# Kernel tuning notes

Hardware: AMD Instinct MI355X
Metric: run time of the kernel (lower is better)

## Reference

```python
import jax, jax.numpy as jnp
import numpy as np

N = 30000      # nodes
E = 300000     # edges (before self-loops)
F_NODE = 32; F_EDGE = 16
HID = 64       # hidden_channels
H = 4; C = 64  # heads, per-head channels (GATConv out_channels = HID)
NEG_SLOPE_ATT = 0.2   # GATConv negative_slope
NEG_SLOPE_ACT = 0.01  # F.leaky_relu default
LN_EPS = 1e-5


def setup_inputs() -> dict:
    key = jax.random.key(0)
    ks = jax.random.split(key, 32)
    def w(k, shape, fan_in):
        return jax.random.normal(k, shape, jnp.float32) * (1.0 / np.sqrt(fan_in))
    inp = {
        "x": jax.random.normal(ks[0], (N, F_NODE), jnp.float32),
        "edge_index": jax.random.randint(ks[1], (2, E), 0, N),
        "edge_attr": jax.random.normal(ks[2], (E, F_EDGE), jnp.float32),
        "wn": w(ks[3], (F_NODE, HID), F_NODE), "bn": jnp.zeros((HID,), jnp.float32),
        "we": w(ks[4], (F_EDGE, HID), F_EDGE), "be": jnp.zeros((HID,), jnp.float32),
    }
    for i, off in ((1, 5), (2, 13)):
        inp[f"lin{i}"] = w(ks[off], (HID, H * C), HID)        # GATConv.lin
        inp[f"line{i}"] = w(ks[off + 1], (HID, H * C), HID)    # GATConv.lin_edge
        inp[f"as{i}"] = w(ks[off + 2], (H, C), C)              # att_src
        inp[f"ad{i}"] = w(ks[off + 3], (H, C), C)              # att_dst
        inp[f"ae{i}"] = w(ks[off + 4], (H, C), C)              # att_edge
        inp[f"b{i}"] = jnp.zeros((C,), jnp.float32)            # GATConv bias (concat=False -> C)
        inp[f"g{i}"] = jnp.ones((HID,), jnp.float32)           # LayerNorm weight
        inp[f"bt{i}"] = jnp.zeros((HID,), jnp.float32)         # LayerNorm bias
    return inp


def layernorm(x, g, b):
    mu = x.mean(-1, keepdims=True)
    v = ((x - mu) ** 2).mean(-1, keepdims=True)
    return (x - mu) / jnp.sqrt(v + LN_EPS) * g + b


def gat_layer(x, src, dst, e_attr, lin_w, lin_e_w, att_src, att_dst, att_edge, bias, n):
    # x: [n, HID]; e_attr: [E2, HID]; edge lists already include self-loops
    E2 = src.shape[0]
    h = (x @ lin_w).reshape(n, H, C)          # [n,H,C]
    e = (e_attr @ lin_e_w).reshape(E2, H, C)  # [E2,H,C]
    a_src = (h * att_src[None]).sum(-1)       # [n,H]
    a_dst = (h * att_dst[None]).sum(-1)       # [n,H]
    a_edge = (e * att_edge[None]).sum(-1)     # [E2,H]
    a = jax.nn.leaky_relu(a_src[src] + a_dst[dst] + a_edge, NEG_SLOPE_ATT)
    # scatter-softmax over destination neighborhoods (every node has a self-loop)
    m = jax.ops.segment_max(a, dst, num_segments=n)
    ex = jnp.exp(a - m[dst])
    den = jax.ops.segment_sum(ex, dst, num_segments=n)
    alpha = ex / den[dst]                     # [E2,H]
    out = jax.ops.segment_sum(h[src] * alpha[..., None], dst, num_segments=n)  # [n,H,C]
    return out.mean(axis=1) + bias, alpha     # concat=False: average heads


def reference(x, edge_index, edge_attr, wn, bn, we, be,
              lin1, line1, as1, ad1, ae1, b1, g1, bt1,
              lin2, line2, as2, ad2, ae2, b2, g2, bt2):
    n = x.shape[0]
    x = jax.nn.relu(x @ wn + bn)
    ea = jax.nn.relu(edge_attr @ we + be)
    src, dst = edge_index[0], edge_index[1]
    # PyG add_self_loops(fill_value='mean'): self-loop edge_attr = mean of incoming edge_attr
    ones = jnp.ones((src.shape[0],), ea.dtype)
    deg = jax.ops.segment_sum(ones, dst, num_segments=n)
    mean_ea = jax.ops.segment_sum(ea, dst, num_segments=n) / jnp.maximum(deg, 1.0)[:, None]
    loop = jnp.arange(n, dtype=src.dtype)
    src_f = jnp.concatenate([src, loop])
    dst_f = jnp.concatenate([dst, loop])
    ea_f = jnp.concatenate([ea, mean_ea], axis=0)
    h1, alpha1 = gat_layer(x, src_f, dst_f, ea_f, lin1, line1, as1, ad1, ae1, b1, n)
    h1 = layernorm(jax.nn.leaky_relu(h1, NEG_SLOPE_ACT), g1, bt1)
    # dropout is identity in eval mode
    h2, alpha2 = gat_layer(h1, src_f, dst_f, ea_f, lin2, line2, as2, ad2, ae2, b2, n)
    h2 = layernorm(jax.nn.leaky_relu(h2, NEG_SLOPE_ACT), g2, bt2)
    return h2, alpha1, alpha2
```

## Files before the change

kernel.cpp:

```cpp
#include <hip/hip_runtime.h>

#define FN 32
#define FE 16
#define HID 64
#define HEADS 4
#define CHC 64

typedef float f32x4 __attribute__((ext_vector_type(4)));

__device__ __forceinline__ float bf2f(unsigned short u) {
  unsigned int x = ((unsigned int)u) << 16;
  return __builtin_bit_cast(float, x);
}
__device__ __forceinline__ unsigned short f2bf(float f) {
  unsigned int x = __builtin_bit_cast(unsigned int, f);
  unsigned int r = (x + 0x7fff + ((x >> 16) & 1)) >> 16;
  return (unsigned short)r;
}
__device__ __forceinline__ unsigned int pack2bf(float a, float b) {
  return (unsigned int)f2bf(a) | ((unsigned int)f2bf(b) << 16);
}

__device__ __forceinline__ void reduce8_store(const float p[8],
    float* __restrict__ arr1, float* __restrict__ arr2, size_t pos, int lane,
    float scale)
{
  float q[4];
  {
    bool hi = lane & 1;
    #pragma unroll
    for (int m = 0; m < 4; m++) {
      float keep = hi ? p[m + 4] : p[m];
      float send = hi ? p[m] : p[m + 4];
      q[m] = keep + __shfl_xor(send, 1);
    }
  }
  float r[2];
  {
    bool hi = lane & 2;
    #pragma unroll
    for (int m = 0; m < 2; m++) {
      float keep = hi ? q[m + 2] : q[m];
      float send = hi ? q[m] : q[m + 2];
      r[m] = keep + __shfl_xor(send, 2);
    }
  }
  float s;
  {
    bool hi = lane & 4;
    float keep = hi ? r[1] : r[0];
    float send = hi ? r[0] : r[1];
    s = keep + __shfl_xor(send, 4);
  }
  s += __shfl_xor(s, 8);
  s += __shfl_xor(s, 16);
  s += __shfl_xor(s, 32);
  if (lane < 8) {
    int entry = ((lane & 1) << 2) | (lane & 2) | ((lane >> 2) & 1);
    if (entry < 4) arr1[pos * 4 + entry] = s * scale;
    else           arr2[pos * 4 + entry - 4] = s * scale;
  }
}

__global__ __launch_bounds__(256) void k_vecs(
    const float* __restrict__ lin1, const float* __restrict__ line1,
    const float* __restrict__ as1, const float* __restrict__ ad1,
    const float* __restrict__ ae1,
    const float* __restrict__ lin2, const float* __restrict__ line2,
    const float* __restrict__ as2, const float* __restrict__ ad2,
    const float* __restrict__ ae2,
    float* __restrict__ vS, float* __restrict__ vD, float* __restrict__ vE)
{
  int bi = blockIdx.x;
  int l = bi / 3, kind = bi % 3;
  const float* lin = (kind == 2) ? (l ? line2 : line1) : (l ? lin2 : lin1);
  const float* att = (kind == 0) ? (l ? as2 : as1)
                   : (kind == 1) ? (l ? ad2 : ad1) : (l ? ae2 : ae1);
  float* out = ((kind == 0) ? vS : (kind == 1) ? vD : vE) + l * 256;
  int t = threadIdx.x;
  int c = t >> 2, hd = t & 3;
  float acc = 0.f;
  for (int cc = 0; cc < CHC; cc++)
    acc += lin[c * (HEADS * CHC) + hd * CHC + cc] * att[hd * CHC + cc];
  out[c * 4 + hd] = acc;
}

__global__ __launch_bounds__(256) void k_x1(const float* __restrict__ x,
    const float* __restrict__ wn, const float* __restrict__ bn,
    const float* __restrict__ vS, const float* __restrict__ vD,
    float* __restrict__ x1, float* __restrict__ ssrc, float* __restrict__ sdst,
    int n)
{
  int t = threadIdx.x; int w = t >> 6; int lane = t & 63;
  int v = blockIdx.x * 4 + w;
  __shared__ float xs[4][FN];
  if (v < n && lane < FN) xs[w][lane] = x[(size_t)v * FN + lane];
  __syncthreads();
  if (v >= n) return;
  float acc = bn[lane];
  #pragma unroll
  for (int k = 0; k < FN; k++) acc += xs[w][k] * wn[k * HID + lane];
  acc = fmaxf(acc, 0.f);
  x1[(size_t)v * HID + lane] = acc;
  float4 s4 = ((const float4*)vS)[lane];
  float4 d4 = ((const float4*)vD)[lane];
  float p[8] = {acc * s4.x, acc * s4.y, acc * s4.z, acc * s4.w,
                acc * d4.x, acc * d4.y, acc * d4.z, acc * d4.w};
  reduce8_store(p, ssrc, sdst, (size_t)v, lane, 1.f);
}

__global__ __launch_bounds__(256) void k_deg(const int* __restrict__ dst,
                                             int* __restrict__ deg, int E)
{
  int e = blockIdx.x * 256 + threadIdx.x;
  if (e < E) atomicAdd(&deg[dst[e]], 1);
}

__global__ __launch_bounds__(1024) void k_scan1(const int* __restrict__ deg,
    int* __restrict__ rowptr, int* __restrict__ bsum, int n)
{
  __shared__ int wsum[16];
  int t = threadIdx.x, wv = t >> 6, lane = t & 63;
  int i = blockIdx.x * 1024 + t;
  int val = (i < n) ? deg[i] : 0;
  int sc = val;
  #pragma unroll
  for (int off = 1; off < 64; off <<= 1) {
    int u = __shfl_up(sc, off);
    if (lane >= off) sc += u;
  }
  if (lane == 63) wsum[wv] = sc;
  __syncthreads();
  int woff = 0;
  #pragma unroll
  for (int k = 0; k < 16; k++) woff += (k < wv) ? wsum[k] : 0;
  if (i < n) rowptr[i] = woff + sc - val;
  if (t == 0) {
    int tot = 0;
    #pragma unroll
    for (int k = 0; k < 16; k++) tot += wsum[k];
    bsum[blockIdx.x] = tot;
  }
}

__global__ __launch_bounds__(1024) void k_scan23(const int* __restrict__ bsum,
    int* __restrict__ rowptr, int nb, int n)
{
  int b = blockIdx.x;
  int t = threadIdx.x;
  int off = 0;
  for (int j = 0; j < b; j++) off += bsum[j];
  int i = b * 1024 + t;
  if (i < n) rowptr[i] += off;
  if (b == 0 && t == 0) {
    int tot = 0;
    for (int j = 0; j < nb; j++) tot += bsum[j];
    rowptr[n] = tot;
  }
}

__global__ __launch_bounds__(256) void k_fill(const int* __restrict__ src,
    const int* __restrict__ dst, const int* __restrict__ rowptr,
    int* __restrict__ cnt, int* __restrict__ eid, int* __restrict__ srcs,
    int* __restrict__ perm, int E)
{
  int e = blockIdx.x * 256 + threadIdx.x;
  if (e < E) {
    int d = dst[e];
    int pos = rowptr[d] + atomicAdd(&cnt[d], 1);
    eid[pos] = e;
    srcs[pos] = src[e];
    perm[e] = pos;
  }
}

__global__ __launch_bounds__(256) void k_aeg_e(const float* __restrict__ eattr,
    const float* __restrict__ we, const float* __restrict__ be,
    const float* __restrict__ vE, const int* __restrict__ perm,
    float* __restrict__ aeg1, float* __restrict__ aeg2, int E)
{
  __shared__ float4 we_t4[HID][4];
  __shared__ float4 vE_s[2][HID];
  __shared__ float  be_s[HID];
  int t = threadIdx.x;
  for (int i = t; i < FE * HID; i += 256) {
    int k = i >> 6, c = i & 63;
    ((float*)we_t4)[c * 16 + k] = we[i];
  }
  for (int i = t; i < 512; i += 256) ((float*)vE_s)[i] = vE[i];
  if (t < HID) be_s[t] = be[t];
  __syncthreads();

  int e = blockIdx.x * 256 + t;
  if (e >= E) return;
  const float4* er = (const float4*)(eattr + (size_t)e * FE);
  float4 A = er[0], B = er[1], C4 = er[2], D = er[3];
  float ta[FE] = {A.x, A.y, A.z, A.w, B.x, B.y, B.z, B.w,
                  C4.x, C4.y, C4.z, C4.w, D.x, D.y, D.z, D.w};
  float4 acc1 = make_float4(0.f, 0.f, 0.f, 0.f);
  float4 acc2 = make_float4(0.f, 0.f, 0.f, 0.f);
  #pragma unroll 4
  for (int c = 0; c < HID; c++) {
    float4 w0 = we_t4[c][0], w1 = we_t4[c][1], w2 = we_t4[c][2], w3 = we_t4[c][3];
    float ea = be_s[c];
    ea += ta[0] * w0.x + ta[1] * w0.y + ta[2] * w0.z + ta[3] * w0.w;
    ea += ta[4] * w1.x + ta[5] * w1.y + ta[6] * w1.z + ta[7] * w1.w;
    ea += ta[8] * w2.x + ta[9] * w2.y + ta[10] * w2.z + ta[11] * w2.w;
    ea += ta[12] * w3.x + ta[13] * w3.y + ta[14] * w3.z + ta[15] * w3.w;
    ea = fmaxf(ea, 0.f);
    float4 u1 = vE_s[0][c], u2 = vE_s[1][c];
    acc1.x += ea * u1.x; acc1.y += ea * u1.y; acc1.z += ea * u1.z; acc1.w += ea * u1.w;
    acc2.x += ea * u2.x; acc2.y += ea * u2.y; acc2.z += ea * u2.z; acc2.w += ea * u2.w;
  }
  int pos = perm[e];
  *(float4*)(aeg1 + (size_t)pos * 4) = acc1;
  *(float4*)(aeg2 + (size_t)pos * 4) = acc2;
}

__global__ __launch_bounds__(256) void k_self_aeg(const int* __restrict__ rowptr,
    float* __restrict__ aeg1, float* __restrict__ aeg2, int E, int n)
{
  int t = threadIdx.x;
  int v = blockIdx.x * 32 + (t >> 3);
  if (v >= n) return;
  int ent = t & 7;
  int h = ent & 3;
  const float* srcp = (ent < 4) ? aeg1 : aeg2;
  int r0 = rowptr[v], r1 = rowptr[v + 1];
  float s = 0.f;
  for (int j = r0; j < r1; j++) s += srcp[(size_t)j * 4 + h];
  float m = s / fmaxf((float)(r1 - r0), 1.f);
  if (ent < 4) aeg1[((size_t)E + v) * 4 + h] = m;
  else         aeg2[((size_t)E + v) * 4 + h] = m;
}

__global__ __launch_bounds__(256) void k_h(const float* __restrict__ xin,
    const float* __restrict__ lin, unsigned short* __restrict__ h_bf, int n)
{
  int t = threadIdx.x, wv = t >> 6, lane = t & 63;
  int v0 = blockIdx.x * 16;
  __shared__ float xs[16][HID];
  {
    int node = t >> 4, ch4 = (t & 15) * 4;
    int vv = v0 + node;
    float4 val = make_float4(0.f, 0.f, 0.f, 0.f);
    if (vv < n) val = *(const float4*)(xin + (size_t)vv * HID + ch4);
    *(float4*)&xs[node][ch4] = val;
  }
  __syncthreads();
  float acc[4][4];
  #pragma unroll
  for (int i = 0; i < 4; i++)
    #pragma unroll
    for (int j = 0; j < 4; j++) acc[i][j] = 0.f;
  const float4* lin4 = (const float4*)lin;
  int nd0 = wv * 4;
  #pragma unroll 4
  for (int kb = 0; kb < 16; kb++) {
    float4 xv[4];
    #pragma unroll
    for (int i = 0; i < 4; i++) xv[i] = *(const float4*)&xs[nd0 + i][kb * 4];
    float4 lv0 = lin4[(kb * 4 + 0) * 64 + lane];
    float4 lv1 = lin4[(kb * 4 + 1) * 64 + lane];
    float4 lv2 = lin4[(kb * 4 + 2) * 64 + lane];
    float4 lv3 = lin4[(kb * 4 + 3) * 64 + lane];
    #pragma unroll
    for (int i = 0; i < 4; i++) {
      acc[i][0] += xv[i].x * lv0.x + xv[i].y * lv1.x + xv[i].z * lv2.x + xv[i].w * lv3.x;
      acc[i][1] += xv[i].x * lv0.y + xv[i].y * lv1.y + xv[i].z * lv2.y + xv[i].w * lv3.y;
      acc[i][2] += xv[i].x * lv0.z + xv[i].y * lv1.z + xv[i].z * lv2.z + xv[i].w * lv3.z;
      acc[i][3] += xv[i].x * lv0.w + xv[i].y * lv1.w + xv[i].z * lv2.w + xv[i].w * lv3.w;
    }
  }
  #pragma unroll
  for (int i = 0; i < 4; i++) {
    int v = v0 + nd0 + i;
    if (v < n) {
      uint2 u;
      u.x = pack2bf(acc[i][0], acc[i][1]);
      u.y = pack2bf(acc[i][2], acc[i][3]);
      *(uint2*)(h_bf + (size_t)v * 256 + lane * 4) = u;
    }
  }
}

template<bool DOTS>
__global__ __launch_bounds__(256) void k_node(
    const unsigned short* __restrict__ h_bf, const float* __restrict__ ssrc,
    const float* __restrict__ sdst, const float* __restrict__ aegc,
    const int* __restrict__ rowptr, const int* __restrict__ eidArr,
    const int* __restrict__ srcs, const float* __restrict__ bias,
    const float* __restrict__ gamma, const float* __restrict__ beta,
    const float* __restrict__ vS2, const float* __restrict__ vD2,
    float* __restrict__ alpha_out, float* __restrict__ xout,
    float* __restrict__ ssrc_o, float* __restrict__ sdst_o, int n, int E)
{
  __shared__ float als[4][4][64];
  __shared__ int   svec[4][64];
  int t = threadIdx.x; int wv = t >> 6, lane = t & 63;
  int v = blockIdx.x * 4 + wv;
  if (v >= n) return;
  int r0 = rowptr[v], r1 = rowptr[v + 1];
  int deg = r1 - r0, ne = deg + 1;
  int coff = lane * 4;
  int hh = lane >> 4;
  float acc0 = 0.f, acc1 = 0.f, acc2 = 0.f, acc3 = 0.f;
  const float4* aeg4 = (const float4*)aegc;
  const float4* ss4p = (const float4*)ssrc;
  float4 sd4 = ((const float4*)sdst)[v];

  if (ne <= 64) {
    int s = v, eo = E + v;
    if (lane < deg) { s = srcs[r0 + lane]; eo = eidArr[r0 + lane]; }
    bool valid = (lane < ne);
    float a0 = -INFINITY, a1 = -INFINITY, a2 = -INFINITY, a3 = -INFINITY;
    if (valid) {
      float4 ae4 = aeg4[(lane < deg) ? (r0 + lane) : (E + v)];
      float4 ss4 = ss4p[s];
      a0 = ss4.x + sd4.x + ae4.x; a0 = (a0 > 0.f) ? a0 : 0.2f * a0;
      a1 = ss4.y + sd4.y + ae4.y; a1 = (a1 > 0.f) ? a1 : 0.2f * a1;
      a2 = ss4.z + sd4.z + ae4.z; a2 = (a2 > 0.f) ? a2 : 0.2f * a2;
      a3 = ss4.w + sd4.w + ae4.w; a3 = (a3 > 0.f) ? a3 : 0.2f * a3;
    }
    float m0, m1, m2, m3;
    {
      bool hi0 = lane & 1;
      float k0 = hi0 ? a2 : a0, s0 = hi0 ? a0 : a2;
      float k1 = hi0 ? a3 : a1, s1 = hi0 ? a1 : a3;
      float q0 = fmaxf(k0, __shfl_xor(s0, 1));
      float q1 = fmaxf(k1, __shfl_xor(s1, 1));
      bool hi1 = lane & 2;
      float k2 = hi1 ? q1 : q0, s2 = hi1 ? q0 : q1;
      float r = fmaxf(k2, __shfl_xor(s2, 2));
      r = fmaxf(r, __shfl_xor(r, 4));
      r = fmaxf(r, __shfl_xor(r, 8));
      r = fmaxf(r, __shfl_xor(r, 16));
      r = fmaxf(r, __shfl_xor(r, 32));
      m0 = __shfl(r, 0); m1 = __shfl(r, 2); m2 = __shfl(r, 1); m3 = __shfl(r, 3);
    }
    float e0 = __expf(a0 - m0), e1 = __expf(a1 - m1);
    float e2 = __expf(a2 - m2), e3 = __expf(a3 - m3);
    float d0, d1, d2, d3;
    {
      bool hi0 = lane & 1;
      float k0 = hi0 ? e2 : e0, s0 = hi0 ? e0 : e2;
      float k1 = hi0 ? e3 : e1, s1 = hi0 ? e1 : e3;
      float q0 = k0 + __shfl_xor(s0, 1);
      float q1 = k1 + __shfl_xor(s1, 1);
      bool hi1 = lane & 2;
      float k2 = hi1 ? q1 : q0, s2 = hi1 ? q0 : q1;
      float r = k2 + __shfl_xor(s2, 2);
      r += __shfl_xor(r, 4);
      r += __shfl_xor(r, 8);
      r += __shfl_xor(r, 16);
      r += __shfl_xor(r, 32);
      d0 = __shfl(r, 0); d1 = __shfl(r, 2); d2 = __shfl(r, 1); d3 = __shfl(r, 3);
    }
    float4 alf = make_float4(e0 / d0, e1 / d1, e2 / d2, e3 / d3);
    if (valid) {
      f32x4 alv = {alf.x, alf.y, alf.z, alf.w};
      __builtin_nontemporal_store(alv, (f32x4*)alpha_out + eo);
    }
    als[wv][0][lane] = alf.x;
    als[wv][1][lane] = alf.y;
    als[wv][2][lane] = alf.z;
    als[wv][3][lane] = alf.w;
    svec[wv][lane] = s;
    __builtin_amdgcn_wave_barrier();
    __builtin_amdgcn_sched_barrier(0);
    const float* alsh = als[wv][hh];
    const int* svp = svec[wv];
    for (int jj = 0; jj < ne; jj += 8) {
      int4 sv0 = *(const int4*)(svp + jj);
      int4 sv1 = *(const int4*)(svp + jj + 4);
      float4 al0 = *(const float4*)(alsh + jj);
      float4 al1 = *(const float4*)(alsh + jj + 4);
      uint2 u0 = *(const uint2*)(h_bf + (size_t)sv0.x * 256 + coff);
      uint2 u1 = *(const uint2*)(h_bf + (size_t)sv0.y * 256 + coff);
      uint2 u2 = *(const uint2*)(h_bf + (size_t)sv0.z * 256 + coff);
      uint2 u3 = *(const uint2*)(h_bf + (size_t)sv0.w * 256 + coff);
      uint2 u4 = *(const uint2*)(h_bf + (size_t)sv1.x * 256 + coff);
      uint2 u5 = *(const uint2*)(h_bf + (size_t)sv1.y * 256 + coff);
      uint2 u6 = *(const uint2*)(h_bf + (size_t)sv1.z * 256 + coff);
      uint2 u7 = *(const uint2*)(h_bf + (size_t)sv1.w * 256 + coff);
      acc0 += al0.x * bf2f((unsigned short)(u0.x & 0xffff))
            + al0.y * bf2f((unsigned short)(u1.x & 0xffff))
            + al0.z * bf2f((unsigned short)(u2.x & 0xffff))
            + al0.w * bf2f((unsigned short)(u3.x & 0xffff))
            + al1.x * bf2f((unsigned short)(u4.x & 0xffff))
            + al1.y * bf2f((unsigned short)(u5.x & 0xffff))
            + al1.z * bf2f((unsigned short)(u6.x & 0xffff))
            + al1.w * bf2f((unsigned short)(u7.x & 0xffff));
      acc1 += al0.x * bf2f((unsigned short)(u0.x >> 16))
            + al0.y * bf2f((unsigned short)(u1.x >> 16))
            + al0.z * bf2f((unsigned short)(u2.x >> 16))
            + al0.w * bf2f((unsigned short)(u3.x >> 16))
            + al1.x * bf2f((unsigned short)(u4.x >> 16))
            + al1.y * bf2f((unsigned short)(u5.x >> 16))
            + al1.z * bf2f((unsigned short)(u6.x >> 16))
            + al1.w * bf2f((unsigned short)(u7.x >> 16));
      acc2 += al0.x * bf2f((unsigned short)(u0.y & 0xffff))
            + al0.y * bf2f((unsigned short)(u1.y & 0xffff))
            + al0.z * bf2f((unsigned short)(u2.y & 0xffff))
            + al0.w * bf2f((unsigned short)(u3.y & 0xffff))
            + al1.x * bf2f((unsigned short)(u4.y & 0xffff))
            + al1.y * bf2f((unsigned short)(u5.y & 0xffff))
            + al1.z * bf2f((unsigned short)(u6.y & 0xffff))
            + al1.w * bf2f((unsigned short)(u7.y & 0xffff));
      acc3 += al0.x * bf2f((unsigned short)(u0.y >> 16))
            + al0.y * bf2f((unsigned short)(u1.y >> 16))
            + al0.z * bf2f((unsigned short)(u2.y >> 16))
            + al0.w * bf2f((unsigned short)(u3.y >> 16))
            + al1.x * bf2f((unsigned short)(u4.y >> 16))
            + al1.y * bf2f((unsigned short)(u5.y >> 16))
            + al1.z * bf2f((unsigned short)(u6.y >> 16))
            + al1.w * bf2f((unsigned short)(u7.y >> 16));
    }
  } else {
    int j4 = lane >> 2, hb = lane & 3;
    float sd = sdst[v * 4 + hb];
    float m = -INFINITY;
    for (int jb = 0; jb < ne; jb += 16) {
      int jc = jb + j4;
      if (jc < ne) {
        int s2 = (jc < deg) ? srcs[r0 + jc] : v;
        float ae = (jc < deg) ? aegc[(size_t)(r0 + jc) * 4 + hb]
                              : aegc[((size_t)E + v) * 4 + hb];
        float a = ssrc[s2 * 4 + hb] + sd + ae;
        a = (a > 0.f) ? a : 0.2f * a;
        m = fmaxf(m, a);
      }
    }
    m = fmaxf(m, __shfl_xor(m, 4));
    m = fmaxf(m, __shfl_xor(m, 8));
    m = fmaxf(m, __shfl_xor(m, 16));
    m = fmaxf(m, __shfl_xor(m, 32));
    float den = 0.f;
    for (int jb = 0; jb < ne; jb += 16) {
      int jc = jb + j4;
      if (jc < ne) {
        int s2 = (jc < deg) ? srcs[r0 + jc] : v;
        float ae = (jc < deg) ? aegc[(size_t)(r0 + jc) * 4 + hb]
                              : aegc[((size_t)E + v) * 4 + hb];
        float a = ssrc[s2 * 4 + hb] + sd + ae;
        a = (a > 0.f) ? a : 0.2f * a;
        den += __expf(a - m);
      }
    }
    den += __shfl_xor(den, 4);
    den += __shfl_xor(den, 8);
    den += __shfl_xor(den, 16);
    den += __shfl_xor(den, 32);
    float rden = 1.f / den;
    for (int jb = 0; jb < ne; jb += 16) {
      int jc = jb + j4;
      if (jc < ne) {
        int s2 = (jc < deg) ? srcs[r0 + jc] : v;
        int eo = (jc < deg) ? eidArr[r0 + jc] : E + v;
        float ae = (jc < deg) ? aegc[(size_t)(r0 + jc) * 4 + hb]
                              : aegc[((size_t)E + v) * 4 + hb];
        float a = ssrc[s2 * 4 + hb] + sd + ae;
        a = (a > 0.f) ? a : 0.2f * a;
        alpha_out[(size_t)eo * 4 + hb] = __expf(a - m) * rden;
      }
    }
    float sdh = __shfl(sd, hh);
    float mh  = __shfl(m, hh);
    float rdh = __shfl(rden, hh);
    for (int jc = 0; jc < ne; jc++) {
      int s0 = (jc < deg) ? srcs[r0 + jc] : v;
      size_t ap = (jc < deg) ? (size_t)(r0 + jc) : (size_t)E + v;
      float a = ssrc[s0 * 4 + hh] + sdh + aegc[ap * 4 + hh];
      a = (a > 0.f) ? a : 0.2f * a;
      float al = __expf(a - mh) * rdh;
      uint2 u = *(const uint2*)(h_bf + (size_t)s0 * 256 + coff);
      acc0 += al * bf2f((unsigned short)(u.x & 0xffff));
      acc1 += al * bf2f((unsigned short)(u.x >> 16));
      acc2 += al * bf2f((unsigned short)(u.y & 0xffff));
      acc3 += al * bf2f((unsigned short)(u.y >> 16));
    }
  }

  acc0 += __shfl_xor(acc0, 16); acc0 += __shfl_xor(acc0, 32);
  acc1 += __shfl_xor(acc1, 16); acc1 += __shfl_xor(acc1, 32);
  acc2 += __shfl_xor(acc2, 16); acc2 += __shfl_xor(acc2, 32);
  acc3 += __shfl_xor(acc3, 16); acc3 += __shfl_xor(acc3, 32);

  int c16 = lane & 15;
  float4 b4 = ((const float4*)bias)[c16];
  float v0 = acc0 * 0.25f + b4.x;
  float v1 = acc1 * 0.25f + b4.y;
  float v2 = acc2 * 0.25f + b4.z;
  float v3 = acc3 * 0.25f + b4.w;
  v0 = (v0 > 0.f) ? v0 : 0.01f * v0;
  v1 = (v1 > 0.f) ? v1 : 0.01f * v1;
  v2 = (v2 > 0.f) ? v2 : 0.01f * v2;
  v3 = (v3 > 0.f) ? v3 : 0.01f * v3;
  float mu = v0 + v1 + v2 + v3;
  mu += __shfl_xor(mu, 1); mu += __shfl_xor(mu, 2);
  mu += __shfl_xor(mu, 4); mu += __shfl_xor(mu, 8);
  mu *= (1.f / 64.f);
  float d0 = v0 - mu, d1 = v1 - mu, d2 = v2 - mu, d3 = v3 - mu;
  float var = d0 * d0 + d1 * d1 + d2 * d2 + d3 * d3;
  var += __shfl_xor(var, 1); var += __shfl_xor(var, 2);
  var += __shfl_xor(var, 4); var += __shfl_xor(var, 8);
  var *= (1.f / 64.f);
  float rstd = rsqrtf(var + 1e-5f);
  float4 g4 = ((const float4*)gamma)[c16];
  float4 be4 = ((const float4*)beta)[c16];
  float y0 = d0 * rstd * g4.x + be4.x;
  float y1 = d1 * rstd * g4.y + be4.y;
  float y2 = d2 * rstd * g4.z + be4.z;
  float y3 = d3 * rstd * g4.w + be4.w;
  if (lane < 16) {
    float4 y = make_float4(y0, y1, y2, y3);
    *(float4*)(xout + (size_t)v * HID + lane * 4) = y;
  }
  if constexpr (DOTS) {
    int c0 = c16 * 4;
    float4 vs0 = ((const float4*)vS2)[c0],     vs1 = ((const float4*)vS2)[c0 + 1];
    float4 vs2 = ((const float4*)vS2)[c0 + 2], vs3 = ((const float4*)vS2)[c0 + 3];
    float4 vd0 = ((const float4*)vD2)[c0],     vd1 = ((const float4*)vD2)[c0 + 1];
    float4 vd2 = ((const float4*)vD2)[c0 + 2], vd3 = ((const float4*)vD2)[c0 + 3];
    float p[8];
    p[0] = y0 * vs0.x + y1 * vs1.x + y2 * vs2.x + y3 * vs3.x;
    p[1] = y0 * vs0.y + y1 * vs1.y + y2 * vs2.y + y3 * vs3.y;
    p[2] = y0 * vs0.z + y1 * vs1.z + y2 * vs2.z + y3 * vs3.z;
    p[3] = y0 * vs0.w + y1 * vs1.w + y2 * vs2.w + y3 * vs3.w;
    p[4] = y0 * vd0.x + y1 * vd1.x + y2 * vd2.x + y3 * vd3.x;
    p[5] = y0 * vd0.y + y1 * vd1.y + y2 * vd2.y + y3 * vd3.y;
    p[6] = y0 * vd0.z + y1 * vd1.z + y2 * vd2.z + y3 * vd3.z;
    p[7] = y0 * vd0.w + y1 * vd1.w + y2 * vd2.w + y3 * vd3.w;
    reduce8_store(p, ssrc_o, sdst_o, (size_t)v, lane, 0.25f);
  }
}

extern "C" void kernel_launch(void* const* d_in, const int* in_sizes, int n_in,
                              void* d_out, int out_size, void* d_ws, size_t ws_size,
                              hipStream_t stream)
{
  const float* x     = (const float*)d_in[0];
  const int*   eidx  = (const int*)d_in[1];
  const float* eattr = (const float*)d_in[2];
  const float* wn    = (const float*)d_in[3];
  const float* bn    = (const float*)d_in[4];
  const float* we    = (const float*)d_in[5];
  const float* be    = (const float*)d_in[6];
  const float* lin1  = (const float*)d_in[7];
  const float* line1 = (const float*)d_in[8];
  const float* as1   = (const float*)d_in[9];
  const float* ad1   = (const float*)d_in[10];
  const float* ae1   = (const float*)d_in[11];
  const float* b1    = (const float*)d_in[12];
  const float* g1    = (const float*)d_in[13];
  const float* bt1   = (const float*)d_in[14];
  const float* lin2  = (const float*)d_in[15];
  const float* line2 = (const float*)d_in[16];
  const float* as2   = (const float*)d_in[17];
  const float* ad2   = (const float*)d_in[18];
  const float* ae2   = (const float*)d_in[19];
  const float* b2    = (const float*)d_in[20];
  const float* g2    = (const float*)d_in[21];
  const float* bt2   = (const float*)d_in[22];

  int n = in_sizes[0] / FN;
  int E = in_sizes[1] / 2;
  const int* srcA = eidx;
  const int* dstA = eidx + E;

  float* out_h2 = (float*)d_out;
  float* alpha1 = out_h2 + (size_t)n * HID;
  float* alpha2 = alpha1 + (size_t)(E + n) * 4;

  char* ws = (char*)d_ws;
  size_t off = 0;
  auto alloc = [&](size_t bytes) -> char* {
    char* p = ws + off;
    off += (bytes + 255) & ~(size_t)255;
    return p;
  };
  unsigned short* h_bf = (unsigned short*)alloc((size_t)n * 256 * 2);
  float* x1      = (float*)alloc((size_t)n * HID * 4);
  float* h1      = (float*)alloc((size_t)n * HID * 4);
  float* aeg1c   = (float*)alloc((size_t)(E + n) * 4 * 4);
  float* aeg2c   = (float*)alloc((size_t)(E + n) * 4 * 4);
  float* ssrc1   = (float*)alloc((size_t)n * 4 * 4);
  float* sdst1   = (float*)alloc((size_t)n * 4 * 4);
  float* ssrc2   = (float*)alloc((size_t)n * 4 * 4);
  float* sdst2   = (float*)alloc((size_t)n * 4 * 4);
  float* vS      = (float*)alloc(512 * 4);
  float* vD      = (float*)alloc(512 * 4);
  float* vE      = (float*)alloc(512 * 4);
  int*   deg     = (int*)alloc((size_t)n * 4);
  int*   cnt     = (int*)alloc((size_t)n * 4);
  int*   rowptr  = (int*)alloc((size_t)(n + 1) * 4);
  int*   eid     = (int*)alloc((size_t)E * 4);
  int*   srcs    = (int*)alloc((size_t)E * 4);
  int*   perm    = (int*)alloc((size_t)E * 4);
  int*   bsum    = (int*)alloc(1024 * 4);

  hipMemsetAsync(deg, 0, (size_t)n * 4, stream);
  hipMemsetAsync(cnt, 0, (size_t)n * 4, stream);

  int nb = (n + 1023) / 1024;
  k_vecs<<<6, 256, 0, stream>>>(lin1, line1, as1, ad1, ae1,
                                lin2, line2, as2, ad2, ae2, vS, vD, vE);
  k_x1<<<(n + 3) / 4, 256, 0, stream>>>(x, wn, bn, vS, vD, x1, ssrc1, sdst1, n);
  k_deg<<<(E + 255) / 256, 256, 0, stream>>>(dstA, deg, E);
  k_scan1<<<nb, 1024, 0, stream>>>(deg, rowptr, bsum, n);
  k_scan23<<<nb, 1024, 0, stream>>>(bsum, rowptr, nb, n);
  k_fill<<<(E + 255) / 256, 256, 0, stream>>>(srcA, dstA, rowptr, cnt, eid, srcs, perm, E);
  k_aeg_e<<<(E + 255) / 256, 256, 0, stream>>>(eattr, we, be, vE, perm, aeg1c, aeg2c, E);
  k_self_aeg<<<(n + 31) / 32, 256, 0, stream>>>(rowptr, aeg1c, aeg2c, E, n);

  k_h<<<(n + 15) / 16, 256, 0, stream>>>(x1, lin1, h_bf, n);
  k_node<true><<<(n + 3) / 4, 256, 0, stream>>>(h_bf, ssrc1, sdst1, aeg1c,
      rowptr, eid, srcs, b1, g1, bt1, vS + 256, vD + 256,
      alpha1, h1, ssrc2, sdst2, n, E);
  k_h<<<(n + 15) / 16, 256, 0, stream>>>(h1, lin2, h_bf, n);
  k_node<false><<<(n + 3) / 4, 256, 0, stream>>>(h_bf, ssrc2, sdst2, aeg2c,
      rowptr, eid, srcs, b2, g2, bt2, nullptr, nullptr,
      alpha2, out_h2, nullptr, nullptr, n, E);
}
```

Before: 223.9 us.

## Fuse input projection into first h GEMM and prefetch neighbor features early

```diff
diff --git a/kernel.cpp b/kernel.cpp
--- a/kernel.cpp
+++ b/kernel.cpp
@@ -19,47 +19,6 @@
 }
 __device__ __forceinline__ unsigned int pack2bf(float a, float b) {
   return (unsigned int)f2bf(a) | ((unsigned int)f2bf(b) << 16);
-}
-
-__device__ __forceinline__ void reduce8_store(const float p[8],
-    float* __restrict__ arr1, float* __restrict__ arr2, size_t pos, int lane,
-    float scale)
-{
-  float q[4];
-  {
-    bool hi = lane & 1;
-    #pragma unroll
-    for (int m = 0; m < 4; m++) {
-      float keep = hi ? p[m + 4] : p[m];
-      float send = hi ? p[m] : p[m + 4];
-      q[m] = keep + __shfl_xor(send, 1);
-    }
-  }
-  float r[2];
-  {
-    bool hi = lane & 2;
-    #pragma unroll
-    for (int m = 0; m < 2; m++) {
-      float keep = hi ? q[m + 2] : q[m];
-      float send = hi ? q[m] : q[m + 2];
-      r[m] = keep + __shfl_xor(send, 2);
-    }
-  }
-  float s;
-  {
-    bool hi = lane & 4;
-    float keep = hi ? r[1] : r[0];
-    float send = hi ? r[0] : r[1];
-    s = keep + __shfl_xor(send, 4);
-  }
-  s += __shfl_xor(s, 8);
-  s += __shfl_xor(s, 16);
-  s += __shfl_xor(s, 32);
-  if (lane < 8) {
-    int entry = ((lane & 1) << 2) | (lane & 2) | ((lane >> 2) & 1);
-    if (entry < 4) arr1[pos * 4 + entry] = s * scale;
-    else           arr2[pos * 4 + entry - 4] = s * scale;
-  }
 }
 
 __global__ __launch_bounds__(256) void k_vecs(
@@ -83,30 +42,6 @@
   for (int cc = 0; cc < CHC; cc++)
     acc += lin[c * (HEADS * CHC) + hd * CHC + cc] * att[hd * CHC + cc];
   out[c * 4 + hd] = acc;
-}
-
-__global__ __launch_bounds__(256) void k_x1(const float* __restrict__ x,
-    const float* __restrict__ wn, const float* __restrict__ bn,
-    const float* __restrict__ vS, const float* __restrict__ vD,
-    float* __restrict__ x1, float* __restrict__ ssrc, float* __restrict__ sdst,
-    int n)
-{
-  int t = threadIdx.x; int w = t >> 6; int lane = t & 63;
-  int v = blockIdx.x * 4 + w;
-  __shared__ float xs[4][FN];
-  if (v < n && lane < FN) xs[w][lane] = x[(size_t)v * FN + lane];
-  __syncthreads();
-  if (v >= n) return;
-  float acc = bn[lane];
-  #pragma unroll
-  for (int k = 0; k < FN; k++) acc += xs[w][k] * wn[k * HID + lane];
-  acc = fmaxf(acc, 0.f);
-  x1[(size_t)v * HID + lane] = acc;
-  float4 s4 = ((const float4*)vS)[lane];
-  float4 d4 = ((const float4*)vD)[lane];
-  float p[8] = {acc * s4.x, acc * s4.y, acc * s4.z, acc * s4.w,
-                acc * d4.x, acc * d4.y, acc * d4.z, acc * d4.w};
-  reduce8_store(p, ssrc, sdst, (size_t)v, lane, 1.f);
 }
 
 __global__ __launch_bounds__(256) void k_deg(const int* __restrict__ dst,
@@ -234,6 +169,102 @@
   else         aeg2[((size_t)E + v) * 4 + h] = m;
 }
 
+__global__ __launch_bounds__(256) void k_hx1(const float* __restrict__ x,
+    const float* __restrict__ wn, const float* __restrict__ bn,
+    const float* __restrict__ vS, const float* __restrict__ vD,
+    const float* __restrict__ lin, unsigned short* __restrict__ h_bf,
+    float* __restrict__ ssrc, float* __restrict__ sdst, int n)
+{
+  int t = threadIdx.x, wv = t >> 6, lane = t & 63;
+  int v0 = blockIdx.x * 16;
+  __shared__ float xin_s[16][FN];
+  __shared__ float xs[16][HID];
+  if (t < 128) {
+    int node = t >> 3, c4 = (t & 7) * 4;
+    int vv = v0 + node;
+    float4 val = make_float4(0.f, 0.f, 0.f, 0.f);
+    if (vv < n) val = *(const float4*)(x + (size_t)vv * FN + c4);
+    *(float4*)&xin_s[node][c4] = val;
+  }
+  __syncthreads();
+  {
+    int nd = t >> 4, cg = t & 15;
+    int vv = v0 + nd;
+    const float4* wn4 = (const float4*)wn;
+    float4 a = ((const float4*)bn)[cg];
+    #pragma unroll 8
+    for (int k = 0; k < FN; k++) {
+      float xv = xin_s[nd][k];
+      float4 w = wn4[k * 16 + cg];
+      a.x += xv * w.x; a.y += xv * w.y; a.z += xv * w.z; a.w += xv * w.w;
+    }
+    a.x = fmaxf(a.x, 0.f); a.y = fmaxf(a.y, 0.f);
+    a.z = fmaxf(a.z, 0.f); a.w = fmaxf(a.w, 0.f);
+    *(float4*)&xs[nd][cg * 4] = a;
+    const float4* vS4 = (const float4*)vS;
+    const float4* vD4 = (const float4*)vD;
+    int c0 = cg * 4;
+    float4 vs0 = vS4[c0], vs1 = vS4[c0 + 1], vs2 = vS4[c0 + 2], vs3 = vS4[c0 + 3];
+    float4 vd0 = vD4[c0], vd1 = vD4[c0 + 1], vd2 = vD4[c0 + 2], vd3 = vD4[c0 + 3];
+    float pS[4], pD[4];
+    pS[0] = a.x * vs0.x + a.y * vs1.x + a.z * vs2.x + a.w * vs3.x;
+    pS[1] = a.x * vs0.y + a.y * vs1.y + a.z * vs2.y + a.w * vs3.y;
+    pS[2] = a.x * vs0.z + a.y * vs1.z + a.z * vs2.z + a.w * vs3.z;
+    pS[3] = a.x * vs0.w + a.y * vs1.w + a.z * vs2.w + a.w * vs3.w;
+    pD[0] = a.x * vd0.x + a.y * vd1.x + a.z * vd2.x + a.w * vd3.x;
+    pD[1] = a.x * vd0.y + a.y * vd1.y + a.z * vd2.y + a.w * vd3.y;
+    pD[2] = a.x * vd0.z + a.y * vd1.z + a.z * vd2.z + a.w * vd3.z;
+    pD[3] = a.x * vd0.w + a.y * vd1.w + a.z * vd2.w + a.w * vd3.w;
+    #pragma unroll
+    for (int off = 1; off < 16; off <<= 1) {
+      #pragma unroll
+      for (int h = 0; h < 4; h++) {
+        pS[h] += __shfl_xor(pS[h], off);
+        pD[h] += __shfl_xor(pD[h], off);
+      }
+    }
+    if (cg == 0 && vv < n) {
+      *(float4*)(ssrc + (size_t)vv * 4) = make_float4(pS[0], pS[1], pS[2], pS[3]);
+      *(float4*)(sdst + (size_t)vv * 4) = make_float4(pD[0], pD[1], pD[2], pD[3]);
+    }
+  }
+  __syncthreads();
+  float acc[4][4];
+  #pragma unroll
+  for (int i = 0; i < 4; i++)
+    #pragma unroll
+    for (int j = 0; j < 4; j++) acc[i][j] = 0.f;
+  const float4* lin4 = (const float4*)lin;
+  int nd0 = wv * 4;
+  #pragma unroll 4
+  for (int kb = 0; kb < 16; kb++) {
+    float4 xv[4];
+    #pragma unroll
+    for (int i = 0; i < 4; i++) xv[i] = *(const float4*)&xs[nd0 + i][kb * 4];
+    float4 lv0 = lin4[(kb * 4 + 0) * 64 + lane];
+    float4 lv1 = lin4[(kb * 4 + 1) * 64 + lane];
+    float4 lv2 = lin4[(kb * 4 + 2) * 64 + lane];
+    float4 lv3 = lin4[(kb * 4 + 3) * 64 + lane];
+    #pragma unroll
+    for (int i = 0; i < 4; i++) {
+      acc[i][0] += xv[i].x * lv0.x + xv[i].y * lv1.x + xv[i].z * lv2.x + xv[i].w * lv3.x;
+      acc[i][1] += xv[i].x * lv0.y + xv[i].y * lv1.y + xv[i].z * lv2.y + xv[i].w * lv3.y;
+      acc[i][2] += xv[i].x * lv0.z + xv[i].y * lv1.z + xv[i].z * lv2.z + xv[i].w * lv3.z;
+      acc[i][3] += xv[i].x * lv0.w + xv[i].y * lv1.w + xv[i].z * lv2.w + xv[i].w * lv3.w;
+    }
+  }
+  #pragma unroll
+  for (int i = 0; i < 4; i++) {
+    int v = v0 + nd0 + i;
+    if (v < n) {
+      uint2 u;
+      u.x = pack2bf(acc[i][0], acc[i][1]);
+      u.y = pack2bf(acc[i][2], acc[i][3]);
+      *(uint2*)(h_bf + (size_t)v * 256 + lane * 4) = u;
+    }
+  }
+}
+
 __global__ __launch_bounds__(256) void k_h(const float* __restrict__ xin,
     const float* __restrict__ lin, unsigned short* __restrict__ h_bf, int n)
 {
@@ -295,8 +326,8 @@
     float* __restrict__ alpha_out, float* __restrict__ xout,
     float* __restrict__ ssrc_o, float* __restrict__ sdst_o, int n, int E)
 {
-  __shared__ float als[4][4][64];
-  __shared__ int   svec[4][64];
+  __shared__ float als[4][4][72];
+  __shared__ int   svec[4][72];
   int t = threadIdx.x; int wv = t >> 6, lane = t & 63;
   int v = blockIdx.x * 4 + wv;
   if (v >= n) return;
@@ -313,10 +344,38 @@
     int s = v, eo = E + v;
     if (lane < deg) { s = srcs[r0 + lane]; eo = eidArr[r0 + lane]; }
     bool valid = (lane < ne);
+    float4 ae4 = aeg4[(lane < deg) ? (r0 + lane) : (E + v)];
+    float4 ss4 = ss4p[s];
+    svec[wv][lane] = s;
+    if (lane < 8) svec[wv][64 + lane] = v;
+    __builtin_amdgcn_wave_barrier();
+    __builtin_amdgcn_sched_barrier(0);
+    uint2 pu[16];
+    {
+      const int* svp = svec[wv];
+      int4 sa = *(const int4*)(svp + 0);
+      int4 sb = *(const int4*)(svp + 4);
+      int4 sc_ = *(const int4*)(svp + 8);
+      int4 se_ = *(const int4*)(svp + 12);
+      pu[0]  = *(const uint2*)(h_bf + (size_t)sa.x * 256 + coff);
+      pu[1]  = *(const uint2*)(h_bf + (size_t)sa.y * 256 + coff);
+      pu[2]  = *(const uint2*)(h_bf + (size_t)sa.z * 256 + coff);
+      pu[3]  = *(const uint2*)(h_bf + (size_t)sa.w * 256 + coff);
+      pu[4]  = *(const uint2*)(h_bf + (size_t)sb.x * 256 + coff);
+      pu[5]  = *(const uint2*)(h_bf + (size_t)sb.y * 256 + coff);
+      pu[6]  = *(const uint2*)(h_bf + (size_t)sb.z * 256 + coff);
+      pu[7]  = *(const uint2*)(h_bf + (size_t)sb.w * 256 + coff);
+      pu[8]  = *(const uint2*)(h_bf + (size_t)sc_.x * 256 + coff);
+      pu[9]  = *(const uint2*)(h_bf + (size_t)sc_.y * 256 + coff);
+      pu[10] = *(const uint2*)(h_bf + (size_t)sc_.z * 256 + coff);
+      pu[11] = *(const uint2*)(h_bf + (size_t)sc_.w * 256 + coff);
+      pu[12] = *(const uint2*)(h_bf + (size_t)se_.x * 256 + coff);
+      pu[13] = *(const uint2*)(h_bf + (size_t)se_.y * 256 + coff);
+      pu[14] = *(const uint2*)(h_bf + (size_t)se_.z * 256 + coff);
+      pu[15] = *(const uint2*)(h_bf + (size_t)se_.w * 256 + coff);
+    }
     float a0 = -INFINITY, a1 = -INFINITY, a2 = -INFINITY, a3 = -INFINITY;
     if (valid) {
-      float4 ae4 = aeg4[(lane < deg) ? (r0 + lane) : (E + v)];
-      float4 ss4 = ss4p[s];
       a0 = ss4.x + sd4.x + ae4.x; a0 = (a0 > 0.f) ? a0 : 0.2f * a0;
       a1 = ss4.y + sd4.y + ae4.y; a1 = (a1 > 0.f) ? a1 : 0.2f * a1;
       a2 = ss4.z + sd4.z + ae4.z; a2 = (a2 > 0.f) ? a2 : 0.2f * a2;
@@ -365,12 +424,33 @@
     als[wv][1][lane] = alf.y;
     als[wv][2][lane] = alf.z;
     als[wv][3][lane] = alf.w;
-    svec[wv][lane] = s;
+    if (lane < 8) {
+      als[wv][0][64 + lane] = 0.f;
+      als[wv][1][64 + lane] = 0.f;
+      als[wv][2][64 + lane] = 0.f;
+      als[wv][3][64 + lane] = 0.f;
+    }
     __builtin_amdgcn_wave_barrier();
     __builtin_amdgcn_sched_barrier(0);
     const float* alsh = als[wv][hh];
+    {
+      float4 al0 = *(const float4*)(alsh + 0);
+      float4 al1 = *(const float4*)(alsh + 4);
+      float4 al2 = *(const float4*)(alsh + 8);
+      float4 al3 = *(const float4*)(alsh + 12);
+      float alr[16] = {al0.x, al0.y, al0.z, al0.w, al1.x, al1.y, al1.z, al1.w,
+                       al2.x, al2.y, al2.z, al2.w, al3.x, al3.y, al3.z, al3.w};
+      #pragma unroll
+      for (int j = 0; j < 16; j++) {
+        float al = alr[j];
+        acc0 += al * bf2f((unsigned short)(pu[j].x & 0xffff));
+        acc1 += al * bf2f((unsigned short)(pu[j].x >> 16));
+        acc2 += al * bf2f((unsigned short)(pu[j].y & 0xffff));
+        acc3 += al * bf2f((unsigned short)(pu[j].y >> 16));
+      }
+    }
     const int* svp = svec[wv];
-    for (int jj = 0; jj < ne; jj += 8) {
+    for (int jj = 16; jj < ne; jj += 8) {
       int4 sv0 = *(const int4*)(svp + jj);
       int4 sv1 = *(const int4*)(svp + jj + 4);
       float4 al0 = *(const float4*)(alsh + jj);
@@ -522,16 +602,27 @@
     float4 vs2 = ((const float4*)vS2)[c0 + 2], vs3 = ((const float4*)vS2)[c0 + 3];
     float4 vd0 = ((const float4*)vD2)[c0],     vd1 = ((const float4*)vD2)[c0 + 1];
     float4 vd2 = ((const float4*)vD2)[c0 + 2], vd3 = ((const float4*)vD2)[c0 + 3];
-    float p[8];
-    p[0] = y0 * vs0.x + y1 * vs1.x + y2 * vs2.x + y3 * vs3.x;
-    p[1] = y0 * vs0.y + y1 * vs1.y + y2 * vs2.y + y3 * vs3.y;
-    p[2] = y0 * vs0.z + y1 * vs1.z + y2 * vs2.z + y3 * vs3.z;
-    p[3] = y0 * vs0.w + y1 * vs1.w + y2 * vs2.w + y3 * vs3.w;
-    p[4] = y0 * vd0.x + y1 * vd1.x + y2 * vd2.x + y3 * vd3.x;
-    p[5] = y0 * vd0.y + y1 * vd1.y + y2 * vd2.y + y3 * vd3.y;
-    p[6] = y0 * vd0.z + y1 * vd1.z + y2 * vd2.z + y3 * vd3.z;
-    p[7] = y0 * vd0.w + y1 * vd1.w + y2 * vd2.w + y3 * vd3.w;
-    reduce8_store(p, ssrc_o, sdst_o, (size_t)v, lane, 0.25f);
+    float pS[4], pD[4];
+    pS[0] = y0 * vs0.x + y1 * vs1.x + y2 * vs2.x + y3 * vs3.x;
+    pS[1] = y0 * vs0.y + y1 * vs1.y + y2 * vs2.y + y3 * vs3.y;
+    pS[2] = y0 * vs0.z + y1 * vs1.z + y2 * vs2.z + y3 * vs3.z;
+    pS[3] = y0 * vs0.w + y1 * vs1.w + y2 * vs2.w + y3 * vs3.w;
+    pD[0] = y0 * vd0.x + y1 * vd1.x + y2 * vd2.x + y3 * vd3.x;
+    pD[1] = y0 * vd0.y + y1 * vd1.y + y2 * vd2.y + y3 * vd3.y;
+    pD[2] = y0 * vd0.z + y1 * vd1.z + y2 * vd2.z + y3 * vd3.z;
+    pD[3] = y0 * vd0.w + y1 * vd1.w + y2 * vd2.w + y3 * vd3.w;
+    #pragma unroll
+    for (int off = 1; off < 16; off <<= 1) {
+      #pragma unroll
+      for (int h = 0; h < 4; h++) {
+        pS[h] += __shfl_xor(pS[h], off);
+        pD[h] += __shfl_xor(pD[h], off);
+      }
+    }
+    if (lane == 0) {
+      *(float4*)(ssrc_o + (size_t)v * 4) = make_float4(pS[0], pS[1], pS[2], pS[3]);
+      *(float4*)(sdst_o + (size_t)v * 4) = make_float4(pD[0], pD[1], pD[2], pD[3]);
+    }
   }
 }
 
@@ -580,7 +671,6 @@
     return p;
   };
   unsigned short* h_bf = (unsigned short*)alloc((size_t)n * 256 * 2);
-  float* x1      = (float*)alloc((size_t)n * HID * 4);
   float* h1      = (float*)alloc((size_t)n * HID * 4);
   float* aeg1c   = (float*)alloc((size_t)(E + n) * 4 * 4);
   float* aeg2c   = (float*)alloc((size_t)(E + n) * 4 * 4);
@@ -605,7 +695,6 @@
   int nb = (n + 1023) / 1024;
   k_vecs<<<6, 256, 0, stream>>>(lin1, line1, as1, ad1, ae1,
                                 lin2, line2, as2, ad2, ae2, vS, vD, vE);
-  k_x1<<<(n + 3) / 4, 256, 0, stream>>>(x, wn, bn, vS, vD, x1, ssrc1, sdst1, n);
   k_deg<<<(E + 255) / 256, 256, 0, stream>>>(dstA, deg, E);
   k_scan1<<<nb, 1024, 0, stream>>>(deg, rowptr, bsum, n);
   k_scan23<<<nb, 1024, 0, stream>>>(bsum, rowptr, nb, n);
@@ -613,7 +702,8 @@
   k_aeg_e<<<(E + 255) / 256, 256, 0, stream>>>(eattr, we, be, vE, perm, aeg1c, aeg2c, E);
   k_self_aeg<<<(n + 31) / 32, 256, 0, stream>>>(rowptr, aeg1c, aeg2c, E, n);
 
-  k_h<<<(n + 15) / 16, 256, 0, stream>>>(x1, lin1, h_bf, n);
+  k_hx1<<<(n + 15) / 16, 256, 0, stream>>>(x, wn, bn, vS, vD, lin1, h_bf,
+                                           ssrc1, sdst1, n);
   k_node<true><<<(n + 3) / 4, 256, 0, stream>>>(h_bf, ssrc1, sdst1, aeg1c,
       rowptr, eid, srcs, b1, g1, bt1, vS + 256, vD + 256,
       alpha1, h1, ssrc2, sdst2, n, E);
```

Result: no change. 226.9 us (+1.4%).
